# Kernel tuning notes

Hardware: AMD Instinct MI355X
Metric: run time of the kernel (lower is better)

The kernel has to match this reference:

```python
import jax, jax.numpy as jnp
import numpy as np

OUT, IN = 4096, 4096
GROUP_SIZE = 128
NUMEL = OUT * IN                 # 16,777,216 int4 values
N_GROUPS = NUMEL // GROUP_SIZE   # 131,072
N_PACKED = NUMEL // 2            # 8,388,608 bytes (stored as int32 0..255)


def _dequantize_int4(q_packed, q_scales, q_zeros):
    """Unpack two 4-bit values per byte, dequant per group, reshape to (OUT, IN)."""
    low = q_packed & 0xF                     # [N_PACKED]
    high = (q_packed >> 4) & 0xF             # [N_PACKED]
    # interleave: flat[2i] = low nibble, flat[2i+1] = high nibble
    q = jnp.stack([low, high], axis=-1).reshape(NUMEL)            # [NUMEL] int
    qg = q.astype(jnp.float32).reshape(N_GROUPS, GROUP_SIZE)      # [G, group]
    w = (qg - q_zeros[:, None]) * q_scales[:, None]
    return w.reshape(OUT, IN)


def setup_inputs() -> dict:
    key = jax.random.key(0)
    k = jax.random.split(key, 6)
    x = jax.random.normal(k[0], (4, 2048, IN), dtype=jnp.float32)
    q_packed = jax.random.randint(k[1], (N_PACKED,), 0, 256, dtype=jnp.int32)
    q_scales = jax.random.uniform(k[2], (N_GROUPS,), dtype=jnp.float32) * 0.02 + 1e-3
    q_zeros = jax.random.uniform(k[3], (N_GROUPS,), dtype=jnp.float32) * 15.0
    delta_weight = jax.random.normal(k[4], (OUT, IN), dtype=jnp.float32) * 0.01
    bias = jax.random.normal(k[5], (OUT,), dtype=jnp.float32)
    return {"x": x, "q_packed": q_packed, "q_scales": q_scales,
            "q_zeros": q_zeros, "delta_weight": delta_weight, "bias": bias}


def reference(x, q_packed, q_scales, q_zeros, delta_weight, bias):
    W = _dequantize_int4(q_packed, q_scales, q_zeros)   # [OUT, IN]
    W_eff = W + delta_weight
    # F.linear: y = x @ W_eff^T + bias
    h = jnp.einsum('bsi,oi->bso', x, W_eff) + bias
    return h
```

## Files before the change

### kernel.cpp

```cpp
#include <hip/hip_runtime.h>


#define M_DIM 8192
#define N_DIM 4096
#define K_DIM 4096
#define NUMEL (N_DIM * K_DIM)

typedef _Float16 half_t;
typedef __attribute__((ext_vector_type(4))) _Float16 half4v;
typedef __attribute__((ext_vector_type(8))) _Float16 half8v;
typedef __attribute__((ext_vector_type(4))) float float4v;
typedef __attribute__((ext_vector_type(4))) int int4v;

#define KTILES 64
#define LDT 72

static __device__ __forceinline__ void gload16(const void* g, void* l) {
    __builtin_amdgcn_global_load_lds(
        (const __attribute__((address_space(1))) void*)g,
        (__attribute__((address_space(3))) void*)l, 16, 0, 0);
}

__global__ __launch_bounds__(256) void k_pack_w(
    const int* __restrict__ qp, const float* __restrict__ sc,
    const float* __restrict__ zr, const float* __restrict__ dwt,
    unsigned char* __restrict__ Wp)
{
    const size_t o = ((size_t)blockIdx.x * 256 + threadIdx.x) << 4;
    const int chunk16 = (int)(o >> 14);
    const int c  = (int)(o >> 10) & 15;
    const int ln = (int)(o >> 4) & 63;
    const int n = (chunk16 >> 6) * 128 + (c >> 1) * 16 + (ln & 15);
    const int k = (chunk16 & 63) * 64 + (c & 1) * 32 + (ln >> 4) * 8;
    const long flat = (long)n * K_DIM + k;
    const int g = n * 32 + (k >> 7);
    const float s = sc[g];
    const float zs = zr[g] * s;
    int4v q4 = *(const int4v*)(qp + (flat >> 1));
    float4v d0 = *(const float4v*)(dwt + flat);
    float4v d1 = *(const float4v*)(dwt + flat + 4);
    float d[8] = {d0[0], d0[1], d0[2], d0[3], d1[0], d1[1], d1[2], d1[3]};
    half8v vh;
#pragma unroll
    for (int j = 0; j < 4; ++j) {
        vh[2*j]   = (half_t)fmaf((float)(q4[j] & 15),        s, d[2*j]   - zs);
        vh[2*j+1] = (half_t)fmaf((float)((q4[j] >> 4) & 15), s, d[2*j+1] - zs);
    }
    *(half8v*)(Wp + o) = vh;
}

__global__ __launch_bounds__(256) void k_pack_x(
    const float* __restrict__ X, unsigned char* __restrict__ Xp)
{
    const size_t o = ((size_t)blockIdx.x * 256 + threadIdx.x) << 4;
    const int chunk16 = (int)(o >> 14);
    const int c  = (int)(o >> 10) & 15;
    const int ln = (int)(o >> 4) & 63;
    const int m = (chunk16 >> 6) * 128 + (c >> 1) * 16 + (ln & 15);
    const int k = (chunk16 & 63) * 64 + (c & 1) * 32 + (ln >> 4) * 8;
    const float* src = X + (size_t)m * K_DIM + k;
    float4v x0 = *(const float4v*)(src);
    float4v x1 = *(const float4v*)(src + 4);
    half8v vh;
    vh[0] = (half_t)x0[0]; vh[1] = (half_t)x0[1];
    vh[2] = (half_t)x0[2]; vh[3] = (half_t)x0[3];
    vh[4] = (half_t)x1[0]; vh[5] = (half_t)x1[1];
    vh[6] = (half_t)x1[2]; vh[7] = (half_t)x1[3];
    *(half8v*)(Xp + o) = vh;
}

#define BARX() do { __builtin_amdgcn_sched_barrier(0); \
                    __builtin_amdgcn_s_barrier(); \
                    __builtin_amdgcn_sched_barrier(0); } while(0)
#define WAITV(N) do { asm volatile("s_waitcnt vmcnt(" #N ")" ::: "memory"); \
                      __builtin_amdgcn_sched_barrier(0); } while(0)

#define READ_A(BUF, F0) do { \
_Pragma("unroll") for (int i_ = 0; i_ < 4; ++i_) \
_Pragma("unroll") for (int ks_ = 0; ks_ < 2; ++ks_) \
        ah[i_][ks_] = *(const half8v*)(&lds[BUF][wm] \
            [((((F0) + i_) * 2 + ks_) << 10) + lane16]); \
    } while(0)

#define READ_B(BUF, DST, J0) do { \
_Pragma("unroll") for (int j_ = 0; j_ < 2; ++j_) \
_Pragma("unroll") for (int ks_ = 0; ks_ < 2; ++ks_) \
        DST[j_][ks_] = *(const half8v*)(&lds[BUF][bhalf] \
            [bq8192 + ((((J0) + j_) * 2 + ks_) << 10) + lane16]); \
    } while(0)

#define MFMA_Q(F0, N0, BREG) do { \
    __builtin_amdgcn_s_setprio(1); \
_Pragma("unroll") for (int i_ = 0; i_ < 4; ++i_) \
_Pragma("unroll") for (int j_ = 0; j_ < 2; ++j_) \
_Pragma("unroll") for (int ks_ = 0; ks_ < 2; ++ks_) \
        acc[(F0)+i_][(N0)+j_] = __builtin_amdgcn_mfma_f32_16x16x32_f16( \
            ah[i_][ks_], BREG[j_][ks_], acc[(F0)+i_][(N0)+j_], 0, 0, 0); \
    __builtin_amdgcn_s_setprio(0); \
} while(0)

__global__ __launch_bounds__(512, 2) void k_gemm8ph(
    const unsigned char* __restrict__ Apk, const unsigned char* __restrict__ Bpk,
    const float* __restrict__ bias, float* __restrict__ Y)
{
    __shared__ __align__(16) unsigned char lds[2][4][16384];

    const int tid  = threadIdx.x;
    const int lane = tid & 63;
    const int wave = tid >> 6;
    const int wm = wave >> 2;
    const int wn = wave & 3;
    const int bhalf = 2 + (wn >> 1);
    const int bq8192 = (wn & 1) << 13;
    const int lane16 = lane << 4;

    const int wg = blockIdx.x;
    const int swg = (wg & 7) * 64 + (wg >> 3);
    const int bn = swg & 15;
    const int bm = swg >> 4;

    auto asrc = [&](int h, int tk) {
        return Apk + ((((size_t)(2 * bm + h)) * KTILES + tk) << 14);
    };
    auto bsrc = [&](int h, int tk) {
        return Bpk + ((((size_t)(2 * bn + h)) * KTILES + tk) << 14);
    };
    auto stageh = [&](int b, int h, const unsigned char* s) {
        unsigned char* d = &lds[b][h][tid << 4];
        gload16(s + (tid << 4), d);
        gload16(s + 8192 + (tid << 4), d + 8192);
    };

    half8v ah[4][2], b01[2][2], b23[2][2];
    float4v acc[8][4];
    const float4v zero4 = {0.f, 0.f, 0.f, 0.f};
#pragma unroll
    for (int i = 0; i < 8; ++i)
#pragma unroll
        for (int j = 0; j < 4; ++j) acc[i][j] = zero4;

    stageh(0, 0, asrc(0, 0)); stageh(0, 1, asrc(1, 0));
    stageh(0, 2, bsrc(0, 0)); stageh(0, 3, bsrc(1, 0));
    stageh(1, 2, bsrc(0, 1)); stageh(1, 3, bsrc(1, 1));
    WAITV(4);
    BARX();

    for (int it = 0; it < 31; ++it) {
        const int t1 = 2 * it + 1, t2 = 2 * it + 2, t3 = 2 * it + 3;
        READ_A(0, 0); READ_B(0, b01, 0);
        stageh(1, 0, asrc(0, t1)); stageh(1, 1, asrc(1, t1));
        MFMA_Q(0, 0, b01);
        READ_B(0, b23, 2);
        MFMA_Q(0, 2, b23);
        READ_A(0, 4);
        BARX();
        MFMA_Q(4, 2, b23);
        stageh(0, 2, bsrc(0, t2)); stageh(0, 3, bsrc(1, t2));
        WAITV(4);
        BARX();
        MFMA_Q(4, 0, b01);
        READ_A(1, 0); READ_B(1, b01, 0);
        stageh(0, 0, asrc(0, t2)); stageh(0, 1, asrc(1, t2));
        MFMA_Q(0, 0, b01);
        READ_B(1, b23, 2);
        MFMA_Q(0, 2, b23);
        READ_A(1, 4);
        BARX();
        MFMA_Q(4, 2, b23);
        stageh(1, 2, bsrc(0, t3)); stageh(1, 3, bsrc(1, t3));
        WAITV(4);
        BARX();
        MFMA_Q(4, 0, b01);
    }

    READ_A(0, 0); READ_B(0, b01, 0);
    stageh(1, 0, asrc(0, 63)); stageh(1, 1, asrc(1, 63));
    BARX(); MFMA_Q(0, 0, b01);
    READ_B(0, b23, 2);
    BARX(); MFMA_Q(0, 2, b23);
    READ_A(0, 4);
    BARX(); MFMA_Q(4, 2, b23);
    WAITV(0);
    BARX(); MFMA_Q(4, 0, b01);
    READ_A(1, 0); READ_B(1, b01, 0);
    BARX(); MFMA_Q(0, 0, b01);
    READ_B(1, b23, 2);
    BARX(); MFMA_Q(0, 2, b23);
    READ_A(1, 4);
    BARX(); MFMA_Q(4, 2, b23);
    MFMA_Q(4, 0, b01);

    const long m0 = (long)bm * 256 + wm * 128;
    const long n0 = (long)bn * 256 + wn * 64;
#pragma unroll
    for (int mf = 0; mf < 8; ++mf) {
        const long row = m0 + mf * 16 + (lane >> 4) * 4;
#pragma unroll
        for (int nf = 0; nf < 4; ++nf) {
            const long col = n0 + nf * 16 + (lane & 15);
            const float b = bias[col];
#pragma unroll
            for (int r = 0; r < 4; ++r)
                __builtin_nontemporal_store(acc[mf][nf][r] + b,
                                            &Y[(row + r) * N_DIM + col]);
        }
    }
}

__global__ __launch_bounds__(256, 2) void k_gemm_fused(
    const float* __restrict__ X, const int* __restrict__ qp,
    const float* __restrict__ sc, const float* __restrict__ zr,
    const float* __restrict__ dwt,
    const float* __restrict__ bias, float* __restrict__ Y)
{
    __shared__ __align__(16) half_t Ah[128 * LDT];
    __shared__ __align__(16) half_t Bh[128 * LDT];

    const int tid  = threadIdx.x;
    const int lane = tid & 63;
    const int wave = tid >> 6;
    const int wm = wave >> 1, wn = wave & 1;
    const int bn = blockIdx.x & 31;
    const int bm = blockIdx.x >> 5;
    const long m0 = (long)bm * 128;
    const long n0 = (long)bn * 128;
    const int fr = lane & 15;
    const int ko = (lane >> 4) * 8;

    const float4v zero4 = {0.f, 0.f, 0.f, 0.f};
    float4v acc[4][4];
#pragma unroll
    for (int i = 0; i < 4; ++i)
#pragma unroll
        for (int j = 0; j < 4; ++j) acc[i][j] = zero4;

    for (int k0 = 0; k0 < K_DIM; k0 += 64) {
        {
            const int ar = tid >> 4;
            const int ac = (tid & 15) * 4;
#pragma unroll
            for (int rr = 0; rr < 8; ++rr) {
                const int row = ar + rr * 16;
                float4v xv = *(const float4v*)(X + (m0 + row) * K_DIM + k0 + ac);
                half4v h;
#pragma unroll
                for (int j = 0; j < 4; ++j) h[j] = (half_t)xv[j];
                *(half4v*)(Ah + row * LDT + ac) = h;
            }
        }
        {
            const int cr = tid >> 3;
            const int cc = (tid & 7) * 8;
#pragma unroll
            for (int rr = 0; rr < 4; ++rr) {
                const int row = cr + rr * 32;
                const long n = n0 + row;
                const int g = (int)(n * 32 + (k0 >> 7));
                const float s = sc[g];
                const float zs = zr[g] * s;
                const long flat = n * K_DIM + k0 + cc;
                int4v q4 = *(const int4v*)(qp + (flat >> 1));
                float4v d0 = *(const float4v*)(dwt + flat);
                float4v d1 = *(const float4v*)(dwt + flat + 4);
                float d[8] = {d0[0], d0[1], d0[2], d0[3], d1[0], d1[1], d1[2], d1[3]};
                half8v vh;
#pragma unroll
                for (int j = 0; j < 4; ++j) {
                    vh[2*j]   = (half_t)fmaf((float)(q4[j] & 15),        s, d[2*j]   - zs);
                    vh[2*j+1] = (half_t)fmaf((float)((q4[j] >> 4) & 15), s, d[2*j+1] - zs);
                }
                *(half8v*)(Bh + row * LDT + cc) = vh;
            }
        }
        __syncthreads();
#pragma unroll
        for (int ks = 0; ks < 2; ++ks) {
            const int kk = ks * 32 + ko;
            half8v a2[4], b2[4];
#pragma unroll
            for (int i = 0; i < 4; ++i) {
                a2[i] = *(const half8v*)(Ah + (wm * 64 + i * 16 + fr) * LDT + kk);
                b2[i] = *(const half8v*)(Bh + (wn * 64 + i * 16 + fr) * LDT + kk);
            }
#pragma unroll
            for (int i = 0; i < 4; ++i)
#pragma unroll
                for (int j = 0; j < 4; ++j)
                    acc[i][j] = __builtin_amdgcn_mfma_f32_16x16x32_f16(
                        a2[i], b2[j], acc[i][j], 0, 0, 0);
        }
        __syncthreads();
    }

#pragma unroll
    for (int i = 0; i < 4; ++i) {
        const long mrow = m0 + wm * 64 + i * 16 + (lane >> 4) * 4;
#pragma unroll
        for (int j = 0; j < 4; ++j) {
            const long col = n0 + wn * 64 + j * 16 + (lane & 15);
            const float b = bias[col];
#pragma unroll
            for (int r = 0; r < 4; ++r)
                Y[(mrow + r) * N_DIM + col] = acc[i][j][r] + b;
        }
    }
}

extern "C" void kernel_launch(void* const* d_in, const int* in_sizes, int n_in,
                              void* d_out, int out_size, void* d_ws, size_t ws_size,
                              hipStream_t stream)
{
    const float* X  = (const float*)d_in[0];
    const int*   qp = (const int*)d_in[1];
    const float* sc = (const float*)d_in[2];
    const float* zr = (const float*)d_in[3];
    const float* dwt = (const float*)d_in[4];
    const float* bs = (const float*)d_in[5];
    float* Y = (float*)d_out;

    const size_t needB = (size_t)N_DIM * K_DIM * 2;
    const size_t needA = (size_t)M_DIM * K_DIM * 2;

    if (ws_size >= needA + needB) {
        unsigned char* Bpk = (unsigned char*)d_ws;
        unsigned char* Apk = Bpk + needB;
        k_pack_w<<<dim3((unsigned)(needB >> 12)), dim3(256), 0, stream>>>(qp, sc, zr, dwt, Bpk);
        k_pack_x<<<dim3((unsigned)(needA >> 12)), dim3(256), 0, stream>>>(X, Apk);
        k_gemm8ph<<<dim3((M_DIM / 256) * (N_DIM / 256)), dim3(512), 0, stream>>>(Apk, Bpk, bs, Y);
    } else {
        k_gemm_fused<<<dim3((M_DIM / 128) * (N_DIM / 128)), dim3(256), 0, stream>>>(
            X, qp, sc, zr, dwt, bs, Y);
    }
}
```

Baseline: 284.4 us.

## Restructure GEMM main loop into four-buffer half-tile windows with vmcnt(0) sync

Replaces the 8-phase ping-pong GEMM schedule with a four-slot LDS ring. Each slot holds a 32-K half tile of A and B, and each window stages the next two half tiles before reading and computing the current two. The window then waits on all loads and does one barrier, replacing the several barriers and partial vmcnt waits per K-tile. This simplifies synchronisation and lengthens the prefetch distance. The cost is a full vmcnt(0) drain every window and a different LDS read pattern, which could expose load latency or cause bank conflicts.

After: 302.4 us. +6.3%, slower.

```diff
diff --git a/kernel.cpp b/kernel.cpp
--- a/kernel.cpp
+++ b/kernel.cpp
@@ -72,66 +72,79 @@
 #define BARX() do { __builtin_amdgcn_sched_barrier(0); \
                     __builtin_amdgcn_s_barrier(); \
                     __builtin_amdgcn_sched_barrier(0); } while(0)
-#define WAITV(N) do { asm volatile("s_waitcnt vmcnt(" #N ")" ::: "memory"); \
+#define WAITV0() do { __builtin_amdgcn_sched_barrier(0); \
+                      asm volatile("s_waitcnt vmcnt(0)" ::: "memory"); \
                       __builtin_amdgcn_sched_barrier(0); } while(0)
 
-#define READ_A(BUF, F0) do { \
+#define STAGE_TILE(BUF, T) do { \
+    const int kt_ = (T) >> 1; \
+    const size_t ko_ = ((size_t)kt_ << 14) + (((T) & 1) << 10) + choff; \
+    gload16(Apk + apan0 + ko_, &lds[BUF][ldsd]); \
+    gload16(Apk + apan1 + ko_, &lds[BUF][ldsd + 8192]); \
+    gload16(Bpk + bpan0 + ko_, &lds[BUF][ldsd + 16384]); \
+    gload16(Bpk + bpan1 + ko_, &lds[BUF][ldsd + 24576]); \
+} while(0)
+
+#define RD_A(BUF, DST, RT0) do { \
 _Pragma("unroll") for (int i_ = 0; i_ < 4; ++i_) \
-_Pragma("unroll") for (int ks_ = 0; ks_ < 2; ++ks_) \
-        ah[i_][ks_] = *(const half8v*)(&lds[BUF][wm] \
-            [((((F0) + i_) * 2 + ks_) << 10) + lane16]); \
-    } while(0)
-
-#define READ_B(BUF, DST, J0) do { \
-_Pragma("unroll") for (int j_ = 0; j_ < 2; ++j_) \
-_Pragma("unroll") for (int ks_ = 0; ks_ < 2; ++ks_) \
-        DST[j_][ks_] = *(const half8v*)(&lds[BUF][bhalf] \
-            [bq8192 + ((((J0) + j_) * 2 + ks_) << 10) + lane16]); \
-    } while(0)
-
-#define MFMA_Q(F0, N0, BREG) do { \
+        DST[i_] = *(const half8v*)(&lds[BUF][awm + (((RT0) + i_) << 10) + lane16]); \
+} while(0)
+
+#define RD_B(BUF, DST) do { \
+_Pragma("unroll") for (int j_ = 0; j_ < 4; ++j_) \
+        DST[j_] = *(const half8v*)(&lds[BUF][16384 + bq + (j_ << 10) + lane16]); \
+} while(0)
+
+#define MFMA16(A0, AR, BR) do { \
     __builtin_amdgcn_s_setprio(1); \
 _Pragma("unroll") for (int i_ = 0; i_ < 4; ++i_) \
-_Pragma("unroll") for (int j_ = 0; j_ < 2; ++j_) \
-_Pragma("unroll") for (int ks_ = 0; ks_ < 2; ++ks_) \
-        acc[(F0)+i_][(N0)+j_] = __builtin_amdgcn_mfma_f32_16x16x32_f16( \
-            ah[i_][ks_], BREG[j_][ks_], acc[(F0)+i_][(N0)+j_], 0, 0, 0); \
+_Pragma("unroll") for (int j_ = 0; j_ < 4; ++j_) \
+        acc[(A0)+i_][j_] = __builtin_amdgcn_mfma_f32_16x16x32_f16( \
+            AR[i_], BR[j_], acc[(A0)+i_][j_], 0, 0, 0); \
     __builtin_amdgcn_s_setprio(0); \
 } while(0)
 
-__global__ __launch_bounds__(512, 2) void k_gemm8ph(
+#define WINDOW(BA, BB, TA, STG) do { \
+    if (STG) { STAGE_TILE((BA)^2, (TA)+2); STAGE_TILE((BB)^2, (TA)+3); } \
+    RD_A(BA, ahA, 0); RD_B(BA, bfA); \
+    MFMA16(0, ahA, bfA); \
+    RD_A(BA, ah2, 4); \
+    MFMA16(4, ah2, bfA); \
+    RD_A(BB, ahB, 0); RD_B(BB, bfB); \
+    MFMA16(0, ahB, bfB); \
+    RD_A(BB, ah2, 4); \
+    MFMA16(4, ah2, bfB); \
+    WAITV0(); BARX(); \
+} while(0)
+
+__global__ __launch_bounds__(512, 2) void k_gemm_win(
     const unsigned char* __restrict__ Apk, const unsigned char* __restrict__ Bpk,
     const float* __restrict__ bias, float* __restrict__ Y)
 {
-    __shared__ __align__(16) unsigned char lds[2][4][16384];
+    __shared__ __align__(16) unsigned char lds[4][32768];
 
     const int tid  = threadIdx.x;
     const int lane = tid & 63;
     const int wave = tid >> 6;
     const int wm = wave >> 2;
     const int wn = wave & 3;
-    const int bhalf = 2 + (wn >> 1);
-    const int bq8192 = (wn & 1) << 13;
+    const int awm = wm * 8192;
+    const int bq  = (wn >> 1) * 8192 + (wn & 1) * 4096;
     const int lane16 = lane << 4;
+    const int ldsd = tid << 4;
+    const size_t choff = ((size_t)(tid >> 6) << 11) + ((tid & 63) << 4);
 
     const int wg = blockIdx.x;
     const int swg = (wg & 7) * 64 + (wg >> 3);
     const int bn = swg & 15;
     const int bm = swg >> 4;
 
-    auto asrc = [&](int h, int tk) {
-        return Apk + ((((size_t)(2 * bm + h)) * KTILES + tk) << 14);
-    };
-    auto bsrc = [&](int h, int tk) {
-        return Bpk + ((((size_t)(2 * bn + h)) * KTILES + tk) << 14);
-    };
-    auto stageh = [&](int b, int h, const unsigned char* s) {
-        unsigned char* d = &lds[b][h][tid << 4];
-        gload16(s + (tid << 4), d);
-        gload16(s + 8192 + (tid << 4), d + 8192);
-    };
-
-    half8v ah[4][2], b01[2][2], b23[2][2];
+    const size_t apan0 = ((size_t)(2 * bm) * KTILES) << 14;
+    const size_t apan1 = ((size_t)(2 * bm + 1) * KTILES) << 14;
+    const size_t bpan0 = ((size_t)(2 * bn) * KTILES) << 14;
+    const size_t bpan1 = ((size_t)(2 * bn + 1) * KTILES) << 14;
+
+    half8v ahA[4], ahB[4], ah2[4], bfA[4], bfB[4];
     float4v acc[8][4];
     const float4v zero4 = {0.f, 0.f, 0.f, 0.f};
 #pragma unroll
@@ -139,56 +152,17 @@
 #pragma unroll
         for (int j = 0; j < 4; ++j) acc[i][j] = zero4;
 
-    stageh(0, 0, asrc(0, 0)); stageh(0, 1, asrc(1, 0));
-    stageh(0, 2, bsrc(0, 0)); stageh(0, 3, bsrc(1, 0));
-    stageh(1, 2, bsrc(0, 1)); stageh(1, 3, bsrc(1, 1));
-    WAITV(4);
+    STAGE_TILE(0, 0); STAGE_TILE(1, 1);
+    WAITV0();
     BARX();
 
     for (int it = 0; it < 31; ++it) {
-        const int t1 = 2 * it + 1, t2 = 2 * it + 2, t3 = 2 * it + 3;
-        READ_A(0, 0); READ_B(0, b01, 0);
-        stageh(1, 0, asrc(0, t1)); stageh(1, 1, asrc(1, t1));
-        MFMA_Q(0, 0, b01);
-        READ_B(0, b23, 2);
-        MFMA_Q(0, 2, b23);
-        READ_A(0, 4);
-        BARX();
-        MFMA_Q(4, 2, b23);
-        stageh(0, 2, bsrc(0, t2)); stageh(0, 3, bsrc(1, t2));
-        WAITV(4);
-        BARX();
-        MFMA_Q(4, 0, b01);
-        READ_A(1, 0); READ_B(1, b01, 0);
-        stageh(0, 0, asrc(0, t2)); stageh(0, 1, asrc(1, t2));
-        MFMA_Q(0, 0, b01);
-        READ_B(1, b23, 2);
-        MFMA_Q(0, 2, b23);
-        READ_A(1, 4);
-        BARX();
-        MFMA_Q(4, 2, b23);
-        stageh(1, 2, bsrc(0, t3)); stageh(1, 3, bsrc(1, t3));
-        WAITV(4);
-        BARX();
-        MFMA_Q(4, 0, b01);
-    }
-
-    READ_A(0, 0); READ_B(0, b01, 0);
-    stageh(1, 0, asrc(0, 63)); stageh(1, 1, asrc(1, 63));
-    BARX(); MFMA_Q(0, 0, b01);
-    READ_B(0, b23, 2);
-    BARX(); MFMA_Q(0, 2, b23);
-    READ_A(0, 4);
-    BARX(); MFMA_Q(4, 2, b23);
-    WAITV(0);
-    BARX(); MFMA_Q(4, 0, b01);
-    READ_A(1, 0); READ_B(1, b01, 0);
-    BARX(); MFMA_Q(0, 0, b01);
-    READ_B(1, b23, 2);
-    BARX(); MFMA_Q(0, 2, b23);
-    READ_A(1, 4);
-    BARX(); MFMA_Q(4, 2, b23);
-    MFMA_Q(4, 0, b01);
+        const int t = it << 2;
+        WINDOW(0, 1, t, 1);
+        WINDOW(2, 3, t + 2, 1);
+    }
+    WINDOW(0, 1, 124, 1);
+    WINDOW(2, 3, 126, 0);
 
     const long m0 = (long)bm * 256 + wm * 128;
     const long n0 = (long)bn * 256 + wn * 64;
@@ -326,7 +300,7 @@
         unsigned char* Apk = Bpk + needB;
         k_pack_w<<<dim3((unsigned)(needB >> 12)), dim3(256), 0, stream>>>(qp, sc, zr, dwt, Bpk);
         k_pack_x<<<dim3((unsigned)(needA >> 12)), dim3(256), 0, stream>>>(X, Apk);
-        k_gemm8ph<<<dim3((M_DIM / 256) * (N_DIM / 256)), dim3(512), 0, stream>>>(Apk, Bpk, bs, Y);
+        k_gemm_win<<<dim3((M_DIM / 256) * (N_DIM / 256)), dim3(512), 0, stream>>>(Apk, Bpk, bs, Y);
     } else {
         k_gemm_fused<<<dim3((M_DIM / 128) * (N_DIM / 128)), dim3(256), 0, stream>>>(
             X, qp, sc, zr, dwt, bs, Y);
```
